# Optimization experiments

Measured on AMD Instinct MI355X. Metric: run time of the kernel, lower is better.

## Reference

```python
import jax, jax.numpy as jnp
import numpy as np

N = 262144
D = 1024
H = 512
B = 512  # number of bags / segments


def setup_inputs() -> dict:
    key = jax.random.key(0)
    k1, k2, k3, k4, k5 = jax.random.split(key, 5)
    x = jax.random.normal(k1, (N, D), dtype=jnp.float32)
    batch = jnp.sort(jax.random.randint(k2, (N,), 0, B, dtype=jnp.int64))
    s1 = 1.0 / np.sqrt(D)
    s3 = 1.0 / np.sqrt(H)
    W1 = jax.random.uniform(k3, (H, D), dtype=jnp.float32, minval=-s1, maxval=s1)
    W2 = jax.random.uniform(k4, (H, D), dtype=jnp.float32, minval=-s1, maxval=s1)
    W3 = jax.random.uniform(k5, (1, H), dtype=jnp.float32, minval=-s3, maxval=s3)
    return {"x": x, "batch": batch, "W1": W1, "W2": W2, "W3": W3}


def reference(x, batch, W1, W2, W3):
    # gated attention logits: tanh(x W1^T) * softmax_over_h(x W2^T) -> W3
    ux = jnp.tanh(x @ W1.T)                       # (n, h)
    vx = jax.nn.softmax(x @ W2.T, axis=1)         # (n, h), Softmax(dim=1)
    alpha = (ux * vx) @ W3.T                      # (n, 1)

    # segment-wise stable softmax over instances within each bag
    a = alpha[:, 0]                               # (n,)
    seg_max = jax.ops.segment_max(a, batch, num_segments=B)   # (B,)
    e = jnp.exp(a - seg_max[batch])               # (n,)
    seg_sum = jax.ops.segment_sum(e, batch, num_segments=B)   # (B,)
    w = e / seg_sum[batch]                        # (n,)

    # weighted segment add-pool: (B, d)
    z = jax.ops.segment_sum(x * w[:, None], batch, num_segments=B)
    return z
```

## Files before the change

### kernel.cpp

```cpp
#include <hip/hip_runtime.h>
#include <stdint.h>

#define N_ROWS 262144
#define D_DIM  1024
#define H_DIM  512
#define N_SEG  512

typedef __attribute__((ext_vector_type(4)))  float  f32x4;
typedef __attribute__((ext_vector_type(16))) float  f32x16;
typedef __attribute__((ext_vector_type(8)))  __bf16 bf16x8;
typedef __attribute__((ext_vector_type(4)))  unsigned short u16x4;
typedef __attribute__((ext_vector_type(8)))  unsigned short u16x8;

static __device__ __forceinline__ unsigned short f2bf(float f) {
  union { float f; uint32_t u; } c; c.f = f;
  return (unsigned short)((c.u + 0x7FFFu + ((c.u >> 16) & 1u)) >> 16);
}
static __device__ __forceinline__ float fast_tanh(float u) {
  return 1.0f - 2.0f / (__expf(2.0f * u) + 1.0f);
}

__global__ void cvt_w(const float* __restrict__ W1, const float* __restrict__ W2,
                      unsigned short* __restrict__ wbf) {
  int gid = blockIdx.x * 256 + threadIdx.x;
  int hi  = gid & 1;
  int col = (gid >> 1) & 511;
  int kk  = (gid >> 10) & 63;
  int m   = gid >> 16;
  const float* src = (m ? W2 : W1) + col * 1024 + kk * 16 + hi * 8;
  u16x8 v;
  #pragma unroll
  for (int e = 0; e < 8; ++e) v[e] = f2bf(src[e]);
  *(u16x8*)(wbf + (size_t)gid * 8) = v;
}

#define ENDBAR() do { \
  asm volatile("s_waitcnt lgkmcnt(0)" ::: "memory"); \
  __builtin_amdgcn_s_barrier(); \
} while (0)

#define KST(BUFOFF, KK, WU1, WU2, WL1, WL2) do { \
  WL1 = *(const bf16x8*)(wbf + w1off + (((KK) + 1) << 13)); \
  WL2 = *(const bf16x8*)(wbf + w2off + (((KK) + 1) << 13)); \
  bf16x8 a0 = *(const bf16x8*)(lds + (BUFOFF) + ((ra0 + (((KK) & 3) << 5)) ^ swz)); \
  bf16x8 a1 = *(const bf16x8*)(lds + (BUFOFF) + ((ra0 + 4096 + (((KK) & 3) << 5)) ^ swz)); \
  __builtin_amdgcn_s_setprio(1); \
  au0 = __builtin_amdgcn_mfma_f32_32x32x16_bf16(a0, WU1, au0, 0, 0, 0); \
  av0 = __builtin_amdgcn_mfma_f32_32x32x16_bf16(a0, WU2, av0, 0, 0, 0); \
  au1 = __builtin_amdgcn_mfma_f32_32x32x16_bf16(a1, WU1, au1, 0, 0, 0); \
  av1 = __builtin_amdgcn_mfma_f32_32x32x16_bf16(a1, WU2, av1, 0, 0, 0); \
  __builtin_amdgcn_s_setprio(0); \
} while (0)

#define PACK4(DSTBYTE, Q) do { \
  u16x4 _v; _v[0]=f2bf(Q[0]); _v[1]=f2bf(Q[1]); _v[2]=f2bf(Q[2]); _v[3]=f2bf(Q[3]); \
  *(u16x4*)(lds + (DSTBYTE)) = _v; \
} while (0)

__launch_bounds__(1024, 4)
__global__ void alpha_kernel(const float* __restrict__ x,
                             const unsigned short* __restrict__ wbf,
                             const float* __restrict__ W3,
                             float* __restrict__ a_out)
{
  __shared__ unsigned char lds[32768 + 12288];
  const int tid  = threadIdx.x;
  const int lane = tid & 63;
  const int wid  = tid >> 6;
  const int l31  = lane & 31;
  const int hi   = lane >> 5;
  const int row0 = blockIdx.x << 6;

  const int sr = tid >> 4;
  const int sc = tid & 15;
  const float* xptr = x + ((size_t)(row0 + sr) << 10) + (sc << 2);
  const uint32_t wbyte = ((uint32_t)((sr << 7) + (sc << 3))) ^ (((uint32_t)(sr & 7)) << 4);

  const int col = (wid << 5) + l31;
  const uint32_t w1off = (uint32_t)((col << 4) + (hi << 3));
  const uint32_t w2off = w1off + 524288u;

  f32x16 au0, au1, av0, av1;
  #pragma unroll
  for (int i = 0; i < 16; ++i) { au0[i]=0.f; au1[i]=0.f; av0[i]=0.f; av1[i]=0.f; }

  const uint32_t swz = (((uint32_t)(l31 & 7)) << 4);
  const uint32_t ra0 = (((uint32_t)l31) << 7) + (((uint32_t)hi) << 4);

  f32x4 xa = *(const f32x4*)xptr;
  f32x4 xb = *(const f32x4*)(xptr + 64);
  PACK4(wbyte, xa);
  bf16x8 WA1 = *(const bf16x8*)(wbf + w1off);
  bf16x8 WA2 = *(const bf16x8*)(wbf + w2off);
  bf16x8 WB1, WB2;
  ENDBAR();

  #pragma unroll 1
  for (int t = 0; t < 16; t += 2) {
    if (t + 2 < 16) xa = *(const f32x4*)(xptr + ((t + 2) << 6));
    PACK4(16384 + wbyte, xb);
    KST(0, t * 4 + 0, WA1, WA2, WB1, WB2);
    KST(0, t * 4 + 1, WB1, WB2, WA1, WA2);
    KST(0, t * 4 + 2, WA1, WA2, WB1, WB2);
    KST(0, t * 4 + 3, WB1, WB2, WA1, WA2);
    ENDBAR();
    if (t + 3 < 16) xb = *(const f32x4*)(xptr + ((t + 3) << 6));
    if (t + 2 < 16) PACK4(wbyte, xa);
    KST(16384, t * 4 + 4, WA1, WA2, WB1, WB2);
    KST(16384, t * 4 + 5, WB1, WB2, WA1, WA2);
    KST(16384, t * 4 + 6, WA1, WA2, WB1, WB2);
    KST(16384, t * 4 + 7, WB1, WB2, WA1, WA2);
    ENDBAR();
  }

  float w3v = W3[col];
  float* redm = (float*)(lds + 32768);
  float* reds = (float*)(lds + 32768 + 4096);
  float* redn = (float*)(lds + 32768 + 8192);

  #pragma unroll
  for (int rf = 0; rf < 2; ++rf) {
    const f32x16 U = rf ? au1 : au0;
    const f32x16 V = rf ? av1 : av0;
    float m_[16];
    #pragma unroll
    for (int r = 0; r < 16; ++r) m_[r] = V[r];
    #pragma unroll
    for (int d = 1; d < 32; d <<= 1)
      #pragma unroll
      for (int r = 0; r < 16; ++r) m_[r] = fmaxf(m_[r], __shfl_xor(m_[r], d));
    float s_[16], n_[16];
    #pragma unroll
    for (int r = 0; r < 16; ++r) {
      float p = __expf(V[r] - m_[r]);
      s_[r] = p;
      n_[r] = fast_tanh(U[r]) * p * w3v;
    }
    #pragma unroll
    for (int d = 1; d < 32; d <<= 1)
      #pragma unroll
      for (int r = 0; r < 16; ++r) { s_[r] += __shfl_xor(s_[r], d); n_[r] += __shfl_xor(n_[r], d); }
    if (l31 == 0) {
      #pragma unroll
      for (int r = 0; r < 16; ++r) {
        int row = rf * 32 + (r & 3) + ((r >> 2) << 3) + (hi << 2);
        redm[(wid << 6) + row] = m_[r];
        reds[(wid << 6) + row] = s_[r];
        redn[(wid << 6) + row] = n_[r];
      }
    }
  }
  __syncthreads();
  if (tid < 64) {
    float m = redm[tid];
    #pragma unroll
    for (int w = 1; w < 16; ++w) m = fmaxf(m, redm[(w << 6) + tid]);
    float s = 0.f, n = 0.f;
    #pragma unroll
    for (int w = 0; w < 16; ++w) {
      float sc2 = __expf(redm[(w << 6) + tid] - m);
      s += reds[(w << 6) + tid] * sc2;
      n += redn[(w << 6) + tid] * sc2;
    }
    a_out[row0 + tid] = n / s;
  }
}

static __device__ __forceinline__ int lower_bound(const int* __restrict__ batch, int key) {
  int lo = 0, hi = N_ROWS;
  while (lo < hi) { int mid = (lo + hi) >> 1; if (batch[mid] < key) lo = mid + 1; else hi = mid; }
  return lo;
}

__global__ void seg_kernel(const float* __restrict__ a, const int* __restrict__ batch,
                           float* __restrict__ w) {
  __shared__ float sm[8];
  int b = blockIdx.x;
  int start = lower_bound(batch, b);
  int end   = lower_bound(batch, b + 1);
  int tid = threadIdx.x;

  float m = -3.4e38f;
  for (int i = start + tid; i < end; i += 256) m = fmaxf(m, a[i]);
  for (int d = 1; d < 64; d <<= 1) m = fmaxf(m, __shfl_xor(m, d));
  if ((tid & 63) == 0) sm[tid >> 6] = m;
  __syncthreads();
  m = fmaxf(fmaxf(sm[0], sm[1]), fmaxf(sm[2], sm[3]));

  float s = 0.f;
  for (int i = start + tid; i < end; i += 256) s += __expf(a[i] - m);
  for (int d = 1; d < 64; d <<= 1) s += __shfl_xor(s, d);
  if ((tid & 63) == 0) sm[4 + (tid >> 6)] = s;
  __syncthreads();
  s = sm[4] + sm[5] + sm[6] + sm[7];

  float rinv = 1.0f / s;
  for (int i = start + tid; i < end; i += 256) w[i] = __expf(a[i] - m) * rinv;
}

__global__ void z_kernel(const float* __restrict__ x, const float* __restrict__ w,
                         const int* __restrict__ batch, float* __restrict__ z) {
  int b = blockIdx.x >> 2, part = blockIdx.x & 3;
  int start = lower_bound(batch, b);
  int end   = lower_bound(batch, b + 1);
  int len = end - start;
  int ps = start + ((len * part) >> 2);
  int pe = start + ((len * (part + 1)) >> 2);
  int col = threadIdx.x << 2;

  f32x4 acc = (f32x4){0.f, 0.f, 0.f, 0.f};
  for (int i = ps; i < pe; ++i) {
    f32x4 xv = *(const f32x4*)(x + ((size_t)i << 10) + col);
    float wi = w[i];
    acc += xv * wi;
  }
  float* zp = z + ((size_t)b << 10) + col;
  atomicAdd(zp + 0, acc[0]);
  atomicAdd(zp + 1, acc[1]);
  atomicAdd(zp + 2, acc[2]);
  atomicAdd(zp + 3, acc[3]);
}

extern "C" void kernel_launch(void* const* d_in, const int* in_sizes, int n_in,
                              void* d_out, int out_size, void* d_ws, size_t ws_size,
                              hipStream_t stream) {
  const float* x     = (const float*)d_in[0];
  const int*   batch = (const int*)d_in[1];
  const float* W1    = (const float*)d_in[2];
  const float* W2    = (const float*)d_in[3];
  const float* W3    = (const float*)d_in[4];
  float* z = (float*)d_out;

  unsigned short* wbf = (unsigned short*)d_ws;
  float* a = (float*)((char*)d_ws + (2u << 20));
  float* w = (float*)((char*)d_ws + (3u << 20));

  (void)hipMemsetAsync(d_out, 0, (size_t)N_SEG * D_DIM * sizeof(float), stream);

  cvt_w<<<512, 256, 0, stream>>>(W1, W2, wbf);

  alpha_kernel<<<N_ROWS / 64, 1024, 0, stream>>>(x, wbf, W3, a);

  seg_kernel<<<N_SEG, 256, 0, stream>>>(a, batch, w);

  z_kernel<<<N_SEG * 4, 256, 0, stream>>>(x, w, batch, z);
}
```

Before: 1.116 ms.

## Retile alpha GEMM waves as 2 row groups by 8 column groups

Each wave now computes 32 rows by 64 columns, using one LDS A fragment against four weight fragments, instead of 64 rows by 32 columns. This halves LDS reads per MFMA. The cost is that each weight fragment is fetched from global memory/L2 by two waves per block, doubling weight traffic. The LDS staging buffers and reduction area also shrink to their actual sizes, and the softmax/tanh epilogue now combines two column fragments per wave before the cross-wave reduction.

```diff
diff --git a/kernel.cpp b/kernel.cpp
--- a/kernel.cpp
+++ b/kernel.cpp
@@ -39,16 +39,19 @@
   __builtin_amdgcn_s_barrier(); \
 } while (0)
 
-#define KST(BUFOFF, KK, WU1, WU2, WL1, WL2) do { \
-  WL1 = *(const bf16x8*)(wbf + w1off + (((KK) + 1) << 13)); \
-  WL2 = *(const bf16x8*)(wbf + w2off + (((KK) + 1) << 13)); \
-  bf16x8 a0 = *(const bf16x8*)(lds + (BUFOFF) + ((ra0 + (((KK) & 3) << 5)) ^ swz)); \
-  bf16x8 a1 = *(const bf16x8*)(lds + (BUFOFF) + ((ra0 + 4096 + (((KK) & 3) << 5)) ^ swz)); \
+#define MF(A, B, C) __builtin_amdgcn_mfma_f32_32x32x16_bf16((A), (B), (C), 0, 0, 0)
+
+#define KST(BUFOFF, KK, U0, U1, U2, U3, L0, L1, L2, L3) do { \
+  L0 = *(const bf16x8*)(wbf + wf0 + (((KK) + 1) << 13)); \
+  L1 = *(const bf16x8*)(wbf + wf1 + (((KK) + 1) << 13)); \
+  L2 = *(const bf16x8*)(wbf + wf2 + (((KK) + 1) << 13)); \
+  L3 = *(const bf16x8*)(wbf + wf3 + (((KK) + 1) << 13)); \
+  bf16x8 a_ = *(const bf16x8*)(lds + (BUFOFF) + ((ra0 + (((KK) & 3) << 5)) ^ swz)); \
   __builtin_amdgcn_s_setprio(1); \
-  au0 = __builtin_amdgcn_mfma_f32_32x32x16_bf16(a0, WU1, au0, 0, 0, 0); \
-  av0 = __builtin_amdgcn_mfma_f32_32x32x16_bf16(a0, WU2, av0, 0, 0, 0); \
-  au1 = __builtin_amdgcn_mfma_f32_32x32x16_bf16(a1, WU1, au1, 0, 0, 0); \
-  av1 = __builtin_amdgcn_mfma_f32_32x32x16_bf16(a1, WU2, av1, 0, 0, 0); \
+  au0 = MF(a_, U0, au0); \
+  au1 = MF(a_, U1, au1); \
+  av0 = MF(a_, U2, av0); \
+  av1 = MF(a_, U3, av1); \
   __builtin_amdgcn_s_setprio(0); \
 } while (0)
 
@@ -63,10 +66,12 @@
                              const float* __restrict__ W3,
                              float* __restrict__ a_out)
 {
-  __shared__ unsigned char lds[32768 + 12288];
+  __shared__ unsigned char lds[16384 + 6144];
   const int tid  = threadIdx.x;
   const int lane = tid & 63;
   const int wid  = tid >> 6;
+  const int cgi  = wid & 7;
+  const int rg   = wid >> 3;
   const int l31  = lane & 31;
   const int hi   = lane >> 5;
   const int row0 = blockIdx.x << 6;
@@ -76,65 +81,68 @@
   const float* xptr = x + ((size_t)(row0 + sr) << 10) + (sc << 2);
   const uint32_t wbyte = ((uint32_t)((sr << 7) + (sc << 3))) ^ (((uint32_t)(sr & 7)) << 4);
 
-  const int col = (wid << 5) + l31;
-  const uint32_t w1off = (uint32_t)((col << 4) + (hi << 3));
-  const uint32_t w2off = w1off + 524288u;
+  const int c0 = (cgi << 6) + l31;
+  const int c1 = c0 + 32;
+  const uint32_t wf0 = (uint32_t)((c0 << 4) + (hi << 3));
+  const uint32_t wf1 = (uint32_t)((c1 << 4) + (hi << 3));
+  const uint32_t wf2 = wf0 + 524288u;
+  const uint32_t wf3 = wf1 + 524288u;
 
   f32x16 au0, au1, av0, av1;
   #pragma unroll
   for (int i = 0; i < 16; ++i) { au0[i]=0.f; au1[i]=0.f; av0[i]=0.f; av1[i]=0.f; }
 
   const uint32_t swz = (((uint32_t)(l31 & 7)) << 4);
-  const uint32_t ra0 = (((uint32_t)l31) << 7) + (((uint32_t)hi) << 4);
+  const uint32_t ra0 = (((uint32_t)rg) << 12) + (((uint32_t)l31) << 7) + (((uint32_t)hi) << 4);
 
   f32x4 xa = *(const f32x4*)xptr;
   f32x4 xb = *(const f32x4*)(xptr + 64);
   PACK4(wbyte, xa);
-  bf16x8 WA1 = *(const bf16x8*)(wbf + w1off);
-  bf16x8 WA2 = *(const bf16x8*)(wbf + w2off);
-  bf16x8 WB1, WB2;
+  bf16x8 WA0 = *(const bf16x8*)(wbf + wf0);
+  bf16x8 WA1 = *(const bf16x8*)(wbf + wf1);
+  bf16x8 WA2 = *(const bf16x8*)(wbf + wf2);
+  bf16x8 WA3 = *(const bf16x8*)(wbf + wf3);
+  bf16x8 WB0, WB1, WB2, WB3;
   ENDBAR();
 
   #pragma unroll 1
   for (int t = 0; t < 16; t += 2) {
     if (t + 2 < 16) xa = *(const f32x4*)(xptr + ((t + 2) << 6));
-    PACK4(16384 + wbyte, xb);
-    KST(0, t * 4 + 0, WA1, WA2, WB1, WB2);
-    KST(0, t * 4 + 1, WB1, WB2, WA1, WA2);
-    KST(0, t * 4 + 2, WA1, WA2, WB1, WB2);
-    KST(0, t * 4 + 3, WB1, WB2, WA1, WA2);
+    PACK4(8192 + wbyte, xb);
+    KST(0, t * 4 + 0, WA0, WA1, WA2, WA3, WB0, WB1, WB2, WB3);
+    KST(0, t * 4 + 1, WB0, WB1, WB2, WB3, WA0, WA1, WA2, WA3);
+    KST(0, t * 4 + 2, WA0, WA1, WA2, WA3, WB0, WB1, WB2, WB3);
+    KST(0, t * 4 + 3, WB0, WB1, WB2, WB3, WA0, WA1, WA2, WA3);
     ENDBAR();
     if (t + 3 < 16) xb = *(const f32x4*)(xptr + ((t + 3) << 6));
     if (t + 2 < 16) PACK4(wbyte, xa);
-    KST(16384, t * 4 + 4, WA1, WA2, WB1, WB2);
-    KST(16384, t * 4 + 5, WB1, WB2, WA1, WA2);
-    KST(16384, t * 4 + 6, WA1, WA2, WB1, WB2);
-    KST(16384, t * 4 + 7, WB1, WB2, WA1, WA2);
+    KST(8192, t * 4 + 4, WA0, WA1, WA2, WA3, WB0, WB1, WB2, WB3);
+    KST(8192, t * 4 + 5, WB0, WB1, WB2, WB3, WA0, WA1, WA2, WA3);
+    KST(8192, t * 4 + 6, WA0, WA1, WA2, WA3, WB0, WB1, WB2, WB3);
+    KST(8192, t * 4 + 7, WB0, WB1, WB2, WB3, WA0, WA1, WA2, WA3);
     ENDBAR();
   }
 
-  float w3v = W3[col];
-  float* redm = (float*)(lds + 32768);
-  float* reds = (float*)(lds + 32768 + 4096);
-  float* redn = (float*)(lds + 32768 + 8192);
-
-  #pragma unroll
-  for (int rf = 0; rf < 2; ++rf) {
-    const f32x16 U = rf ? au1 : au0;
-    const f32x16 V = rf ? av1 : av0;
-    float m_[16];
-    #pragma unroll
-    for (int r = 0; r < 16; ++r) m_[r] = V[r];
+  float w3a = W3[c0];
+  float w3b = W3[c1];
+  float* redm = (float*)(lds + 16384);
+  float* reds = redm + 512;
+  float* redn = redm + 1024;
+
+  {
+    float m_[16], s_[16], n_[16];
+    #pragma unroll
+    for (int r = 0; r < 16; ++r) m_[r] = fmaxf(av0[r], av1[r]);
     #pragma unroll
     for (int d = 1; d < 32; d <<= 1)
       #pragma unroll
       for (int r = 0; r < 16; ++r) m_[r] = fmaxf(m_[r], __shfl_xor(m_[r], d));
-    float s_[16], n_[16];
     #pragma unroll
     for (int r = 0; r < 16; ++r) {
-      float p = __expf(V[r] - m_[r]);
-      s_[r] = p;
-      n_[r] = fast_tanh(U[r]) * p * w3v;
+      float p0 = __expf(av0[r] - m_[r]);
+      float p1 = __expf(av1[r] - m_[r]);
+      s_[r] = p0 + p1;
+      n_[r] = fast_tanh(au0[r]) * p0 * w3a + fast_tanh(au1[r]) * p1 * w3b;
     }
     #pragma unroll
     for (int d = 1; d < 32; d <<= 1)
@@ -143,10 +151,10 @@
     if (l31 == 0) {
       #pragma unroll
       for (int r = 0; r < 16; ++r) {
-        int row = rf * 32 + (r & 3) + ((r >> 2) << 3) + (hi << 2);
-        redm[(wid << 6) + row] = m_[r];
-        reds[(wid << 6) + row] = s_[r];
-        redn[(wid << 6) + row] = n_[r];
+        int row = (rg << 5) + (r & 3) + ((r >> 2) << 3) + (hi << 2);
+        redm[(cgi << 6) + row] = m_[r];
+        reds[(cgi << 6) + row] = s_[r];
+        redn[(cgi << 6) + row] = n_[r];
       }
     }
   }
@@ -154,13 +162,13 @@
   if (tid < 64) {
     float m = redm[tid];
     #pragma unroll
-    for (int w = 1; w < 16; ++w) m = fmaxf(m, redm[(w << 6) + tid]);
+    for (int c = 1; c < 8; ++c) m = fmaxf(m, redm[(c << 6) + tid]);
     float s = 0.f, n = 0.f;
     #pragma unroll
-    for (int w = 0; w < 16; ++w) {
-      float sc2 = __expf(redm[(w << 6) + tid] - m);
-      s += reds[(w << 6) + tid] * sc2;
-      n += redn[(w << 6) + tid] * sc2;
+    for (int c = 0; c < 8; ++c) {
+      float sc2 = __expf(redm[(c << 6) + tid] - m);
+      s += reds[(c << 6) + tid] * sc2;
+      n += redn[(c << 6) + tid] * sc2;
     }
     a_out[row0 + tid] = n / s;
   }
```

New measurement: 1.129 ms. Within noise of the previous version (+1.2%).
